# Performance work log

Measured on AMD Instinct MI355X. Metric: run time of the kernel, lower is better.

## Reference

```python
import jax, jax.numpy as jnp
import numpy as np

WS = 8
NH = 6

def _ln(x, g, b, eps=1e-5):
    m = x.mean(-1, keepdims=True)
    v = jnp.var(x, axis=-1, keepdims=True)
    return (x - m) / jnp.sqrt(v + eps) * g + b

def _dwconv(x_nchw, k):
    # depthwise 3x3, stride 1, padding 1 (SAME); k: (C,1,3,3)
    return jax.lax.conv_general_dilated(
        x_nchw, k, (1, 1), 'SAME',
        dimension_numbers=('NCHW', 'OIHW', 'NCHW'),
        feature_group_count=x_nchw.shape[1])

def setup_inputs() -> dict:
    key = jax.random.key(0)
    ks = jax.random.split(key, 12)
    B, H, W, C = 2, 256, 256, 180
    hd_ffn = 360
    s = 0.02
    return {
        'x': jax.random.normal(ks[0], (B, H * W, C), jnp.float32),
        'w_qkv': jax.random.normal(ks[1], (3 * C, C), jnp.float32) * s,
        'b_rel': jax.random.normal(ks[2], (NH, WS * WS, WS * WS), jnp.float32) * s,
        'w_proj': jax.random.normal(ks[3], (C, C), jnp.float32) * s,
        'b_proj': jnp.zeros((C,), jnp.float32),
        'conv_dw': jax.random.normal(ks[4], (C, 1, 3, 3), jnp.float32) * 0.1,
        'cg_w1': jax.random.normal(ks[5], (C // 8, C), jnp.float32) * s,
        'cg_w2': jax.random.normal(ks[6], (C, C // 8), jnp.float32) * s,
        'ffn_w1': jax.random.normal(ks[7], (hd_ffn, C), jnp.float32) * s,
        'ffn_dw': jax.random.normal(ks[8], (hd_ffn, 1, 3, 3), jnp.float32) * 0.1,
        'ffn_w2': jax.random.normal(ks[9], (C, hd_ffn), jnp.float32) * s,
        'n1_g': jnp.ones((C,), jnp.float32),
        'n1_b': jnp.zeros((C,), jnp.float32),
        'n2_g': jnp.ones((C,), jnp.float32),
        'n2_b': jnp.zeros((C,), jnp.float32),
        'H': H,
        'W': W,
    }

def reference(x, w_qkv, b_rel, w_proj, b_proj, conv_dw, cg_w1, cg_w2,
              ffn_w1, ffn_dw, ffn_w2, n1_g, n1_b, n2_g, n2_b, H, W):
    B, L, C = x.shape
    hd = C // NH
    scale = hd ** -0.5
    n1 = _ln(x, n1_g, n1_b)
    # --- spatial window attention branch ---
    xw = n1.reshape(B, H // WS, WS, W // WS, WS, C)
    xw = xw.transpose(0, 1, 3, 2, 4, 5).reshape(-1, WS * WS, C)  # (nw, 64, C)
    qkv = (xw @ w_qkv.T).reshape(-1, WS * WS, 3, NH, hd).transpose(2, 0, 3, 1, 4)
    q, k, v = qkv[0], qkv[1], qkv[2]  # (nw, nh, 64, hd)
    attn = jax.nn.softmax((q * scale) @ jnp.swapaxes(k, -2, -1) + b_rel, axis=-1)
    out = (attn @ v).transpose(0, 2, 1, 3).reshape(-1, WS * WS, C)
    out = out @ w_proj.T + b_proj
    attn_feat = out.reshape(B, H // WS, W // WS, WS, WS, C)
    attn_feat = attn_feat.transpose(0, 1, 3, 2, 4, 5).reshape(B, L, C)
    # --- conv branch: depthwise 3x3 + GELU ---
    nchw = n1.transpose(0, 2, 1).reshape(B, C, H, W)
    conv_feat = jax.nn.gelu(_dwconv(nchw, conv_dw), approximate=False)
    conv_feat = conv_feat.reshape(B, C, L).transpose(0, 2, 1)
    # --- AIM: channel gate on conv_feat modulates attn_feat ---
    pooled = conv_feat.mean(axis=1)  # (B, C) == AdaptiveAvgPool2d(1)
    cm = jax.nn.sigmoid(jax.nn.gelu(pooled @ cg_w1.T, approximate=False) @ cg_w2.T)
    x = x + (attn_feat * cm[:, None, :] + conv_feat)
    # --- FFN with depthwise spatial mixing ---
    n2 = _ln(x, n2_g, n2_b)
    h = jax.nn.gelu(n2 @ ffn_w1.T, approximate=False)  # (B, L, hd_ffn)
    hdim = h.shape[-1]
    h_s = _dwconv(h.transpose(0, 2, 1).reshape(B, hdim, H, W), ffn_dw)
    h_s = h_s.reshape(B, hdim, L).transpose(0, 2, 1)
    return x + h_s @ ffn_w2.T
```

## Files before the change

### kernel.cpp

```cpp
#include <hip/hip_runtime.h>
#include <hip/hip_bf16.h>
#include <math.h>

#define BATCH 2
#define IMG 256
#define LTOK 65536
#define CH 180
#define BL (BATCH * LTOK)
#define HDF 360

using frag_ab = __attribute__((ext_vector_type(8))) short;
using frag_cd = __attribute__((ext_vector_type(4))) float;

__device__ __forceinline__ float b2f(unsigned short u) {
    union { unsigned int i; float f; } v; v.i = ((unsigned int)u) << 16; return v.f;
}
__device__ __forceinline__ float blo(unsigned int u) {
    union { unsigned int i; float f; } v; v.i = u << 16; return v.f;
}
__device__ __forceinline__ float bhi(unsigned int u) {
    union { unsigned int i; float f; } v; v.i = u & 0xffff0000u; return v.f;
}
__device__ __forceinline__ unsigned short f2b(float f) {
    union { float f; unsigned int i; } v; v.f = f;
    unsigned int x = v.i;
    unsigned int r = (x + 0x7fffu + ((x >> 16) & 1u)) >> 16;
    return (unsigned short)r;
}
__device__ __forceinline__ float gelu_f(float x) {
    return 0.5f * x * (1.0f + erff(x * 0.70710678118654752f));
}

template <int PERM>
__device__ __forceinline__ int perm_row(int row) {
    if (PERM == 1) {
        int b = row >> 16, l = row & 65535;
        int y = l >> 8, x = l & 255;
        return (b << 16) + ((((y >> 3) << 5) + (x >> 3)) << 6) + ((y & 7) << 3) + (x & 7);
    } else if (PERM == 2) {
        int b = row >> 16, wv = row & 65535;
        int wid = wv >> 6, t = wv & 63;
        int wy = wid >> 5, wx = wid & 31;
        return (b << 16) + ((((wy << 3) + (t >> 3))) << 8) + (wx << 3) + (t & 7);
    }
    return row;
}

__global__ __launch_bounds__(256) void convw_kernel(
    const float* __restrict__ a, const float* __restrict__ b,
    const float* __restrict__ c, const float* __restrict__ d,
    const float* __restrict__ cdw, const float* __restrict__ fdw,
    unsigned short* __restrict__ wbf, float* __restrict__ wT1, float* __restrict__ wT2)
{
    int g = blockIdx.x * 256 + threadIdx.x;
    if (g < 259200) {
        float v;
        if      (g < 97200)  v = a[g];
        else if (g < 129600) v = b[g - 97200];
        else if (g < 194400) v = c[g - 129600];
        else                 v = d[g - 194400];
        wbf[g] = f2b(v);
    } else if (g < 265680) {
        int i = g - 259200;
        int tap = i / 180, ch = i % 180;
        wT1[i] = cdw[ch * 9 + tap];
    } else if (g < 278640) {
        int i = g - 265680;
        int tap = i / 360, ch = i % 360;
        wT2[i] = fdw[ch * 9 + tap];
    }
}

__device__ __forceinline__ void ld4(const float* p, float v[4]) {
    float4 t = *(const float4*)p; v[0]=t.x; v[1]=t.y; v[2]=t.z; v[3]=t.w;
}
__device__ __forceinline__ void ld4(const unsigned short* p, float v[4]) {
    ushort4 t = *(const ushort4*)p; v[0]=b2f(t.x); v[1]=b2f(t.y); v[2]=b2f(t.z); v[3]=b2f(t.w);
}

template <typename TIN>
__global__ __launch_bounds__(256) void ln_kernel(
    const TIN* __restrict__ x, const float* __restrict__ g,
    const float* __restrict__ bta, unsigned short* __restrict__ out)
{
    int wave = threadIdx.x >> 6, lane = threadIdx.x & 63;
    int tok = blockIdx.x * 4 + wave;
    const bool act = lane < 45;
    float v[4] = {0.f, 0.f, 0.f, 0.f};
    const TIN* row = x + (size_t)tok * CH;
    if (act) ld4(row + lane * 4, v);
    float s  = v[0] + v[1] + v[2] + v[3];
    float sq = v[0]*v[0] + v[1]*v[1] + v[2]*v[2] + v[3]*v[3];
    #pragma unroll
    for (int off = 32; off > 0; off >>= 1) {
        s  += __shfl_xor(s, off);
        sq += __shfl_xor(sq, off);
    }
    float mean = s * (1.f / CH);
    float var  = sq * (1.f / CH) - mean * mean;
    float rstd = rsqrtf(var + 1e-5f);
    if (act) {
        float4 gg = *(const float4*)&g[lane * 4];
        float4 bb = *(const float4*)&bta[lane * 4];
        unsigned int o0 = (unsigned int)f2b((v[0]-mean)*rstd*gg.x + bb.x)
                        | ((unsigned int)f2b((v[1]-mean)*rstd*gg.y + bb.y) << 16);
        unsigned int o1 = (unsigned int)f2b((v[2]-mean)*rstd*gg.z + bb.z)
                        | ((unsigned int)f2b((v[3]-mean)*rstd*gg.w + bb.w) << 16);
        *(uint2*)(out + (size_t)tok * CH + lane * 4) = make_uint2(o0, o1);
    }
}

__device__ __forceinline__ void stv(float* p, float v) { *p = v; }
__device__ __forceinline__ void stv(unsigned short* p, float v) { *p = f2b(v); }

template <int ACT, bool HAS_BIAS, bool HAS_RES, int PERM, typename TOUT>
__global__ __launch_bounds__(256) void gemm_kernel(
    const unsigned short* __restrict__ X, int ldx,
    const unsigned short* __restrict__ Wt,
    const float* __restrict__ bias,
    const unsigned short* __restrict__ res, int ldr,
    TOUT* __restrict__ Y, int ldy,
    int N, int K)
{
    __shared__ unsigned short Xs[64][40];
    __shared__ unsigned short Ws[64][40];
    const int tid = threadIdx.x;
    const int wave = tid >> 6;
    const int lane = tid & 63;
    const int l16 = lane & 15;
    const int q = lane >> 4;
    const int m0 = blockIdx.x * 64;
    const int n0 = blockIdx.y * 64;
    const int lr = tid >> 2;
    const int lk = (tid & 3) << 3;

    frag_cd acc[4];
    #pragma unroll
    for (int i = 0; i < 4; ++i) acc[i] = (frag_cd){0.f, 0.f, 0.f, 0.f};

    for (int k0 = 0; k0 < K; k0 += 32) {
        const bool kfull = (k0 + 32 <= K);
        {
            const unsigned short* p = X + (size_t)(m0 + lr) * ldx + (k0 + lk);
            if (kfull) {
                *(uint2*)&Xs[lr][lk]     = *(const uint2*)p;
                *(uint2*)&Xs[lr][lk + 4] = *(const uint2*)(p + 4);
            } else {
                #pragma unroll
                for (int j = 0; j < 8; ++j)
                    Xs[lr][lk + j] = (k0 + lk + j < K) ? p[j] : (unsigned short)0;
            }
        }
        {
            const int n = n0 + lr;
            const unsigned short* p = Wt + (size_t)n * K + (k0 + lk);
            if (n < N && kfull) {
                *(uint2*)&Ws[lr][lk]     = *(const uint2*)p;
                *(uint2*)&Ws[lr][lk + 4] = *(const uint2*)(p + 4);
            } else {
                #pragma unroll
                for (int j = 0; j < 8; ++j)
                    Ws[lr][lk + j] = (n < N && (k0 + lk + j) < K) ? p[j] : (unsigned short)0;
            }
        }
        __syncthreads();
        frag_ab bfr = *(const frag_ab*)&Ws[wave * 16 + l16][q * 8];
        #pragma unroll
        for (int mb = 0; mb < 4; ++mb) {
            frag_ab afr = *(const frag_ab*)&Xs[mb * 16 + l16][q * 8];
            acc[mb] = __builtin_amdgcn_mfma_f32_16x16x32_bf16(afr, bfr, acc[mb], 0, 0, 0);
        }
        __syncthreads();
    }
    const int col = n0 + wave * 16 + l16;
    if (col < N) {
        float bv = 0.f;
        if (HAS_BIAS) bv = bias[col];
        #pragma unroll
        for (int mb = 0; mb < 4; ++mb) {
            #pragma unroll
            for (int r = 0; r < 4; ++r) {
                int row = m0 + mb * 16 + q * 4 + r;
                int orow = perm_row<PERM>(row);
                float v = acc[mb][r] + bv;
                if (ACT == 1) v = gelu_f(v);
                if (HAS_RES) v += b2f(res[(size_t)orow * ldr + col]);
                stv(&Y[(size_t)orow * ldy + col], v);
            }
        }
    }
}

__global__ __launch_bounds__(64) void attn_kernel(
    const unsigned short* __restrict__ qkvw,
    const float* __restrict__ b_rel,
    unsigned short* __restrict__ attn_out)
{
    __shared__ float kv[64][36];
    const int blk = blockIdx.x;
    const int h = blk % 6;
    const int w = blk / 6;
    const int lane = threadIdx.x;
    const float scale = 0.18257418583505536f;

    const unsigned short* qrow = qkvw + (size_t)(w * 64 + lane) * 540 + h * 30;

    float q[30];
    #pragma unroll
    for (int d = 0; d < 15; ++d) {
        unsigned int u = *(const unsigned int*)(qrow + 2 * d);
        q[2 * d] = blo(u); q[2 * d + 1] = bhi(u);
    }
    #pragma unroll
    for (int d = 0; d < 15; ++d) {
        unsigned int u = *(const unsigned int*)(qrow + 180 + 2 * d);
        kv[lane][2 * d] = blo(u); kv[lane][2 * d + 1] = bhi(u);
    }
    __syncthreads();

    float s[64];
    const float* br = b_rel + h * 4096 + lane * 64;
    #pragma unroll
    for (int j = 0; j < 64; ++j) {
        const float* kj = &kv[j][0];
        float acc = 0.f;
        #pragma unroll
        for (int d = 0; d < 30; ++d) acc += q[d] * kj[d];
        s[j] = acc * scale + br[j];
    }

    float mx = -1e30f;
    #pragma unroll
    for (int j = 0; j < 64; ++j) mx = fmaxf(mx, s[j]);
    float sum = 0.f;
    #pragma unroll
    for (int j = 0; j < 64; ++j) { s[j] = __expf(s[j] - mx); sum += s[j]; }
    float inv = 1.f / sum;

    __syncthreads();
    #pragma unroll
    for (int d = 0; d < 15; ++d) {
        unsigned int u = *(const unsigned int*)(qrow + 360 + 2 * d);
        kv[lane][2 * d] = blo(u); kv[lane][2 * d + 1] = bhi(u);
    }
    __syncthreads();

    float o[30];
    #pragma unroll
    for (int d = 0; d < 30; ++d) o[d] = 0.f;
    #pragma unroll
    for (int j = 0; j < 64; ++j) {
        const float* vj = &kv[j][0];
        float p = s[j];
        #pragma unroll
        for (int d = 0; d < 30; ++d) o[d] += p * vj[d];
    }
    unsigned short* orow = attn_out + (size_t)(w * 64 + lane) * CH + h * 30;
    #pragma unroll
    for (int d = 0; d < 15; ++d) {
        unsigned int u = (unsigned int)f2b(o[2 * d] * inv)
                       | ((unsigned int)f2b(o[2 * d + 1] * inv) << 16);
        *(unsigned int*)(orow + 2 * d) = u;
    }
}

template <int C, bool DO_GELU>
__global__ __launch_bounds__(256) void dwconv_kernel(
    const unsigned short* __restrict__ in, const float* __restrict__ wT,
    unsigned short* __restrict__ out)
{
    constexpr int NG = (C + 7) / 8;
    constexpr int TY = 8;
    int gid = blockIdx.x * 256 + threadIdx.x;
    int cg = gid % NG;
    int t  = gid / NG;
    int x  = t % IMG;
    int t2 = t / IMG;
    int yb = t2 & 31;
    int bi = t2 >> 5;
    if (bi >= BATCH) return;
    const int c0 = cg * 8;
    const int y0 = yb * TY;

    float w9[9][8];
    #pragma unroll
    for (int tp = 0; tp < 9; ++tp) {
        float4 wa = *(const float4*)&wT[tp * C + c0];
        float4 wb = *(const float4*)&wT[tp * C + c0 + 4];
        w9[tp][0]=wa.x; w9[tp][1]=wa.y; w9[tp][2]=wa.z; w9[tp][3]=wa.w;
        w9[tp][4]=wb.x; w9[tp][5]=wb.y; w9[tp][6]=wb.z; w9[tp][7]=wb.w;
    }

    unsigned int rr[3][3][4];

    auto load_row = [&](int y, unsigned int dst[3][4]) {
        if ((unsigned)y >= (unsigned)IMG) {
            #pragma unroll
            for (int cc = 0; cc < 3; ++cc)
                #pragma unroll
                for (int k = 0; k < 4; ++k) dst[cc][k] = 0u;
            return;
        }
        size_t base = ((size_t)((bi << 16) + (y << 8) + x)) * C + c0;
        #pragma unroll
        for (int cc = 0; cc < 3; ++cc) {
            int xx = x + cc - 1;
            if ((unsigned)xx >= (unsigned)IMG) {
                dst[cc][0] = dst[cc][1] = dst[cc][2] = dst[cc][3] = 0u;
                continue;
            }
            const unsigned short* p = in + base + (ptrdiff_t)(cc - 1) * C;
            uint2 u0 = *(const uint2*)p;
            uint2 u1 = *(const uint2*)(p + 4);
            dst[cc][0] = u0.x; dst[cc][1] = u0.y; dst[cc][2] = u1.x; dst[cc][3] = u1.y;
        }
    };

    load_row(y0 - 1, rr[0]);
    load_row(y0,     rr[1]);

    #pragma unroll
    for (int dy = 0; dy < TY; ++dy) {
        load_row(y0 + dy + 1, rr[(dy + 2) % 3]);
        float acc[8];
        #pragma unroll
        for (int j = 0; j < 8; ++j) acc[j] = 0.f;
        #pragma unroll
        for (int ky = 0; ky < 3; ++ky) {
            unsigned int (*row)[4] = rr[(dy + ky) % 3];
            #pragma unroll
            for (int kx = 0; kx < 3; ++kx) {
                const float* wp = w9[ky * 3 + kx];
                const unsigned int* u = row[kx];
                acc[0] += blo(u[0]) * wp[0];
                acc[1] += bhi(u[0]) * wp[1];
                acc[2] += blo(u[1]) * wp[2];
                acc[3] += bhi(u[1]) * wp[3];
                acc[4] += blo(u[2]) * wp[4];
                acc[5] += bhi(u[2]) * wp[5];
                acc[6] += blo(u[3]) * wp[6];
                acc[7] += bhi(u[3]) * wp[7];
            }
        }
        if (DO_GELU) {
            #pragma unroll
            for (int j = 0; j < 8; ++j) acc[j] = gelu_f(acc[j]);
        }
        size_t ob = ((size_t)((bi << 16) + ((y0 + dy) << 8) + x)) * C + c0;
        unsigned int o0 = (unsigned int)f2b(acc[0]) | ((unsigned int)f2b(acc[1]) << 16);
        unsigned int o1 = (unsigned int)f2b(acc[2]) | ((unsigned int)f2b(acc[3]) << 16);
        *(uint2*)(out + ob) = make_uint2(o0, o1);
        if (c0 + 8 <= C) {
            unsigned int o2 = (unsigned int)f2b(acc[4]) | ((unsigned int)f2b(acc[5]) << 16);
            unsigned int o3 = (unsigned int)f2b(acc[6]) | ((unsigned int)f2b(acc[7]) << 16);
            *(uint2*)(out + ob + 4) = make_uint2(o2, o3);
        }
    }
}

__global__ __launch_bounds__(64) void pool_kernel(
    const unsigned short* __restrict__ cf, float* __restrict__ pooled)
{
    int t = threadIdx.x;
    if (t >= 45) return;
    int b = blockIdx.x >> 7;
    int chunk = blockIdx.x & 127;
    const unsigned short* base = cf + (size_t)(b * LTOK + chunk * 512) * CH + t * 4;
    float s0 = 0.f, s1 = 0.f, s2 = 0.f, s3 = 0.f;
    for (int i = 0; i < 512; ++i) {
        ushort4 v = *(const ushort4*)(base + (size_t)i * CH);
        s0 += b2f(v.x); s1 += b2f(v.y); s2 += b2f(v.z); s3 += b2f(v.w);
    }
    atomicAdd(&pooled[b * CH + t * 4 + 0], s0);
    atomicAdd(&pooled[b * CH + t * 4 + 1], s1);
    atomicAdd(&pooled[b * CH + t * 4 + 2], s2);
    atomicAdd(&pooled[b * CH + t * 4 + 3], s3);
}

__global__ __launch_bounds__(256) void cm_kernel(
    const float* __restrict__ pooled, const float* __restrict__ w1,
    const float* __restrict__ w2, float* __restrict__ cm)
{
    __shared__ float p[BATCH][CH];
    __shared__ float g1[BATCH][22];
    int t = threadIdx.x;
    for (int idx = t; idx < BATCH * CH; idx += 256)
        p[idx / CH][idx % CH] = pooled[idx] * (1.f / (float)LTOK);
    __syncthreads();
    if (t < BATCH * 22) {
        int b = t / 22, u = t % 22;
        float s = 0.f;
        for (int c = 0; c < CH; ++c) s += p[b][c] * w1[u * CH + c];
        g1[b][u] = gelu_f(s);
    }
    __syncthreads();
    for (int idx = t; idx < BATCH * CH; idx += 256) {
        int b = idx / CH, c = idx % CH;
        float s = 0.f;
        for (int u = 0; u < 22; ++u) s += g1[b][u] * w2[c * 22 + u];
        cm[idx] = 1.f / (1.f + __expf(-s));
    }
}

__global__ __launch_bounds__(256) void resid_kernel(
    const float* __restrict__ x, const unsigned short* __restrict__ attn_feat,
    const unsigned short* __restrict__ conv_feat, const float* __restrict__ cm,
    unsigned short* __restrict__ x_mid)
{
    int gid = blockIdx.x * 256 + threadIdx.x;
    int c4 = gid % 45;
    int b = gid / (LTOK * 45);
    float4 xv = ((const float4*)x)[gid];
    ushort4 a = ((const ushort4*)attn_feat)[gid];
    ushort4 c = ((const ushort4*)conv_feat)[gid];
    float4 m = *(const float4*)&cm[b * CH + c4 * 4];
    unsigned int o0 = (unsigned int)f2b(xv.x + b2f(a.x) * m.x + b2f(c.x))
                    | ((unsigned int)f2b(xv.y + b2f(a.y) * m.y + b2f(c.y)) << 16);
    unsigned int o1 = (unsigned int)f2b(xv.z + b2f(a.z) * m.z + b2f(c.z))
                    | ((unsigned int)f2b(xv.w + b2f(a.w) * m.w + b2f(c.w)) << 16);
    ((uint2*)x_mid)[gid] = make_uint2(o0, o1);
}

extern "C" void kernel_launch(void* const* d_in, const int* in_sizes, int n_in,
                              void* d_out, int out_size, void* d_ws, size_t ws_size,
                              hipStream_t stream)
{
    const float* x       = (const float*)d_in[0];
    const float* w_qkv   = (const float*)d_in[1];
    const float* b_rel   = (const float*)d_in[2];
    const float* w_proj  = (const float*)d_in[3];
    const float* b_proj  = (const float*)d_in[4];
    const float* conv_dw = (const float*)d_in[5];
    const float* cg_w1   = (const float*)d_in[6];
    const float* cg_w2   = (const float*)d_in[7];
    const float* ffn_w1  = (const float*)d_in[8];
    const float* ffn_dw  = (const float*)d_in[9];
    const float* ffn_w2  = (const float*)d_in[10];
    const float* n1_g    = (const float*)d_in[11];
    const float* n1_b    = (const float*)d_in[12];
    const float* n2_g    = (const float*)d_in[13];
    const float* n2_b    = (const float*)d_in[14];

    char* ws = (char*)d_ws;
    unsigned short* n1        = (unsigned short*)(ws);
    unsigned short* qkvw      = (unsigned short*)(ws + 47185920);
    unsigned short* conv_feat = (unsigned short*)(ws + 188743680);
    unsigned short* attn_out  = (unsigned short*)(ws);
    unsigned short* attn_feat = (unsigned short*)(ws + 47185920);
    unsigned short* x_mid     = (unsigned short*)(ws + 94371840);
    unsigned short* n2        = (unsigned short*)(ws + 141557760);
    unsigned short* h         = (unsigned short*)(ws);
    unsigned short* h_s       = (unsigned short*)(ws + 141557760);
    float*          pooled    = (float*)(ws + 235929600);
    float*          cmv       = (float*)(ws + 235931040);
    unsigned short* wbf       = (unsigned short*)(ws + 235932480);
    float*          wT1       = (float*)(ws + 236450880);
    float*          wT2       = (float*)(ws + 236476800);
    unsigned short* wqkv_b  = wbf;
    unsigned short* wproj_b = wbf + 97200;
    unsigned short* wffn1_b = wbf + 129600;
    unsigned short* wffn2_b = wbf + 194400;
    float* out = (float*)d_out;

    hipMemsetAsync(pooled, 0, 2880, stream);

    convw_kernel<<<1089, 256, 0, stream>>>(w_qkv, w_proj, ffn_w1, ffn_w2,
                                           conv_dw, ffn_dw, wbf, wT1, wT2);
    ln_kernel<float><<<BL / 4, 256, 0, stream>>>(x, n1_g, n1_b, n1);
    gemm_kernel<0, false, false, 1, unsigned short><<<dim3(BL / 64, 9), 256, 0, stream>>>(
        n1, CH, wqkv_b, nullptr, nullptr, 0, qkvw, 540, 540, CH);
    dwconv_kernel<CH, true><<<1472, 256, 0, stream>>>(n1, wT1, conv_feat);
    pool_kernel<<<BATCH * 128, 64, 0, stream>>>(conv_feat, pooled);
    cm_kernel<<<1, 256, 0, stream>>>(pooled, cg_w1, cg_w2, cmv);
    attn_kernel<<<2048 * 6, 64, 0, stream>>>(qkvw, b_rel, attn_out);
    gemm_kernel<0, true, false, 2, unsigned short><<<dim3(BL / 64, 3), 256, 0, stream>>>(
        attn_out, CH, wproj_b, b_proj, nullptr, 0, attn_feat, CH, CH, CH);
    resid_kernel<<<(BL * CH / 4) / 256, 256, 0, stream>>>(x, attn_feat, conv_feat, cmv, x_mid);
    ln_kernel<unsigned short><<<BL / 4, 256, 0, stream>>>(x_mid, n2_g, n2_b, n2);
    gemm_kernel<1, false, false, 0, unsigned short><<<dim3(BL / 64, 6), 256, 0, stream>>>(
        n2, CH, wffn1_b, nullptr, nullptr, 0, h, HDF, HDF, CH);
    dwconv_kernel<HDF, false><<<2880, 256, 0, stream>>>(h, wT2, h_s);
    gemm_kernel<0, false, true, 0, float><<<dim3(BL / 64, 3), 256, 0, stream>>>(
        h_s, HDF, wffn2_b, nullptr, x_mid, CH, out, CH, CH, HDF);
}
```

Baseline: 1.063 ms.

## Compute window attention with bf16 MFMA and pre-swizzled relative bias

Rewrites the per-window attention kernel to compute QK^T and PV using 16x16x32 bf16 MFMA instructions instead of scalar FP32 dot products, with the softmax done in the MFMA accumulator layout using cross-lane shuffles. The relative position bias is converted once to bf16 and permuted into the accumulator fragment layout in the weight-conversion kernel, so each thread loads its bias values with wide vector loads. Probabilities are rounded to bf16 before the PV product and the bias is held at bf16 precision, which loosens accuracy slightly. The head dimension of 30 is zero-padded to 32 for the MFMA.

```diff
diff --git a/kernel.cpp b/kernel.cpp
--- a/kernel.cpp
+++ b/kernel.cpp
@@ -50,7 +50,9 @@
     const float* __restrict__ a, const float* __restrict__ b,
     const float* __restrict__ c, const float* __restrict__ d,
     const float* __restrict__ cdw, const float* __restrict__ fdw,
-    unsigned short* __restrict__ wbf, float* __restrict__ wT1, float* __restrict__ wT2)
+    const float* __restrict__ brel,
+    unsigned short* __restrict__ wbf, float* __restrict__ wT1, float* __restrict__ wT2,
+    unsigned short* __restrict__ br3)
 {
     int g = blockIdx.x * 256 + threadIdx.x;
     if (g < 259200) {
@@ -68,6 +70,16 @@
         int i = g - 265680;
         int tap = i / 360, ch = i % 360;
         wT2[i] = fdw[ch * 9 + tap];
+    } else if (g < 303216) {
+        int i = g - 278640;
+        int h = i >> 12;
+        int rem = i & 4095;
+        int lane = rem >> 6;
+        int j = rem & 63;
+        int mt = j >> 4, nt = (j >> 2) & 3, r = j & 3;
+        int row = mt * 16 + (lane >> 4) * 4 + r;
+        int col = nt * 16 + (lane & 15);
+        br3[i] = f2b(brel[h * 4096 + row * 64 + col]);
     }
 }
 
@@ -193,74 +205,132 @@
 
 __global__ __launch_bounds__(64) void attn_kernel(
     const unsigned short* __restrict__ qkvw,
-    const float* __restrict__ b_rel,
+    const unsigned short* __restrict__ br3,
     unsigned short* __restrict__ attn_out)
 {
-    __shared__ float kv[64][36];
+    __shared__ unsigned short Pl[64][72];
+    __shared__ unsigned short VT[32][72];
     const int blk = blockIdx.x;
     const int h = blk % 6;
     const int w = blk / 6;
     const int lane = threadIdx.x;
+    const int l16 = lane & 15;
+    const int g4 = lane >> 4;
     const float scale = 0.18257418583505536f;
 
-    const unsigned short* qrow = qkvw + (size_t)(w * 64 + lane) * 540 + h * 30;
-
-    float q[30];
-    #pragma unroll
-    for (int d = 0; d < 15; ++d) {
-        unsigned int u = *(const unsigned int*)(qrow + 2 * d);
-        q[2 * d] = blo(u); q[2 * d + 1] = bhi(u);
-    }
-    #pragma unroll
-    for (int d = 0; d < 15; ++d) {
-        unsigned int u = *(const unsigned int*)(qrow + 180 + 2 * d);
-        kv[lane][2 * d] = blo(u); kv[lane][2 * d + 1] = bhi(u);
+    const unsigned short* base = qkvw + (size_t)w * (64 * 540) + h * 30;
+
+    frag_ab qf[4], kf[4];
+    #pragma unroll
+    for (int t = 0; t < 4; ++t) {
+        const unsigned short* pq = base + (size_t)(t * 16 + l16) * 540 + g4 * 8;
+        union { frag_ab f; uint2 u[2]; } tq, tk;
+        tq.u[0] = *(const uint2*)pq;        tq.u[1] = *(const uint2*)(pq + 4);
+        tk.u[0] = *(const uint2*)(pq + 180); tk.u[1] = *(const uint2*)(pq + 184);
+        if (g4 == 3) { tk.f[6] = 0; tk.f[7] = 0; }
+        qf[t] = tq.f; kf[t] = tk.f;
+    }
+
+    unsigned int brw[32];
+    {
+        const unsigned short* bp = br3 + ((size_t)h << 12) + lane * 64;
+        #pragma unroll
+        for (int c2 = 0; c2 < 8; ++c2)
+            *(uint4*)&brw[c2 * 4] = *(const uint4*)(bp + c2 * 8);
+    }
+
+    frag_cd s[4][4];
+    #pragma unroll
+    for (int mt = 0; mt < 4; ++mt)
+        #pragma unroll
+        for (int nt = 0; nt < 4; ++nt)
+            s[mt][nt] = (frag_cd){0.f, 0.f, 0.f, 0.f};
+    #pragma unroll
+    for (int mt = 0; mt < 4; ++mt)
+        #pragma unroll
+        for (int nt = 0; nt < 4; ++nt)
+            s[mt][nt] = __builtin_amdgcn_mfma_f32_16x16x32_bf16(qf[mt], kf[nt], s[mt][nt], 0, 0, 0);
+
+    {
+        const unsigned short* pv = base + (size_t)lane * 540 + 360;
+        #pragma unroll
+        for (int d2 = 0; d2 < 15; ++d2) {
+            unsigned int u = *(const unsigned int*)(pv + 2 * d2);
+            VT[2 * d2][lane]     = (unsigned short)(u & 0xffffu);
+            VT[2 * d2 + 1][lane] = (unsigned short)(u >> 16);
+        }
+        VT[30][lane] = 0; VT[31][lane] = 0;
+    }
+
+    float inv[4][4];
+    #pragma unroll
+    for (int mt = 0; mt < 4; ++mt) {
+        #pragma unroll
+        for (int r = 0; r < 4; ++r) {
+            float a0 = s[mt][0][r] * scale + (((0 * 4 + r) & 1) ? bhi(brw[(mt * 16 + 0 + r) >> 1]) : blo(brw[(mt * 16 + 0 + r) >> 1]));
+            float a1 = s[mt][1][r] * scale + (((1 * 4 + r) & 1) ? bhi(brw[(mt * 16 + 4 + r) >> 1]) : blo(brw[(mt * 16 + 4 + r) >> 1]));
+            float a2 = s[mt][2][r] * scale + (((2 * 4 + r) & 1) ? bhi(brw[(mt * 16 + 8 + r) >> 1]) : blo(brw[(mt * 16 + 8 + r) >> 1]));
+            float a3 = s[mt][3][r] * scale + (((3 * 4 + r) & 1) ? bhi(brw[(mt * 16 + 12 + r) >> 1]) : blo(brw[(mt * 16 + 12 + r) >> 1]));
+            float m = fmaxf(fmaxf(a0, a1), fmaxf(a2, a3));
+            m = fmaxf(m, __shfl_xor(m, 1));
+            m = fmaxf(m, __shfl_xor(m, 2));
+            m = fmaxf(m, __shfl_xor(m, 4));
+            m = fmaxf(m, __shfl_xor(m, 8));
+            float e0 = __expf(a0 - m), e1 = __expf(a1 - m);
+            float e2 = __expf(a2 - m), e3 = __expf(a3 - m);
+            float sum = e0 + e1 + e2 + e3;
+            sum += __shfl_xor(sum, 1);
+            sum += __shfl_xor(sum, 2);
+            sum += __shfl_xor(sum, 4);
+            sum += __shfl_xor(sum, 8);
+            inv[mt][r] = 1.f / sum;
+            int row = mt * 16 + g4 * 4 + r;
+            Pl[row][l16]      = f2b(e0);
+            Pl[row][16 + l16] = f2b(e1);
+            Pl[row][32 + l16] = f2b(e2);
+            Pl[row][48 + l16] = f2b(e3);
+        }
     }
     __syncthreads();
 
-    float s[64];
-    const float* br = b_rel + h * 4096 + lane * 64;
-    #pragma unroll
-    for (int j = 0; j < 64; ++j) {
-        const float* kj = &kv[j][0];
-        float acc = 0.f;
-        #pragma unroll
-        for (int d = 0; d < 30; ++d) acc += q[d] * kj[d];
-        s[j] = acc * scale + br[j];
-    }
-
-    float mx = -1e30f;
-    #pragma unroll
-    for (int j = 0; j < 64; ++j) mx = fmaxf(mx, s[j]);
-    float sum = 0.f;
-    #pragma unroll
-    for (int j = 0; j < 64; ++j) { s[j] = __expf(s[j] - mx); sum += s[j]; }
-    float inv = 1.f / sum;
-
-    __syncthreads();
-    #pragma unroll
-    for (int d = 0; d < 15; ++d) {
-        unsigned int u = *(const unsigned int*)(qrow + 360 + 2 * d);
-        kv[lane][2 * d] = blo(u); kv[lane][2 * d + 1] = bhi(u);
-    }
-    __syncthreads();
-
-    float o[30];
-    #pragma unroll
-    for (int d = 0; d < 30; ++d) o[d] = 0.f;
-    #pragma unroll
-    for (int j = 0; j < 64; ++j) {
-        const float* vj = &kv[j][0];
-        float p = s[j];
-        #pragma unroll
-        for (int d = 0; d < 30; ++d) o[d] += p * vj[d];
-    }
-    unsigned short* orow = attn_out + (size_t)(w * 64 + lane) * CH + h * 30;
-    #pragma unroll
-    for (int d = 0; d < 15; ++d) {
-        unsigned int u = (unsigned int)f2b(o[2 * d] * inv)
-                       | ((unsigned int)f2b(o[2 * d + 1] * inv) << 16);
-        *(unsigned int*)(orow + 2 * d) = u;
+    frag_ab pf[4][2];
+    #pragma unroll
+    for (int mt = 0; mt < 4; ++mt)
+        #pragma unroll
+        for (int kt = 0; kt < 2; ++kt)
+            pf[mt][kt] = *(const frag_ab*)&Pl[mt * 16 + l16][kt * 32 + g4 * 8];
+    frag_ab vf[2][2];
+    #pragma unroll
+    for (int nt = 0; nt < 2; ++nt)
+        #pragma unroll
+        for (int kt = 0; kt < 2; ++kt)
+            vf[nt][kt] = *(const frag_ab*)&VT[nt * 16 + l16][kt * 32 + g4 * 8];
+
+    frag_cd o[4][2];
+    #pragma unroll
+    for (int mt = 0; mt < 4; ++mt)
+        #pragma unroll
+        for (int nt = 0; nt < 2; ++nt)
+            o[mt][nt] = (frag_cd){0.f, 0.f, 0.f, 0.f};
+    #pragma unroll
+    for (int mt = 0; mt < 4; ++mt)
+        #pragma unroll
+        for (int nt = 0; nt < 2; ++nt)
+            #pragma unroll
+            for (int kt = 0; kt < 2; ++kt)
+                o[mt][nt] = __builtin_amdgcn_mfma_f32_16x16x32_bf16(pf[mt][kt], vf[nt][kt], o[mt][nt], 0, 0, 0);
+
+    unsigned short* ob = attn_out + (size_t)w * (64 * CH) + h * 30;
+    #pragma unroll
+    for (int mt = 0; mt < 4; ++mt) {
+        #pragma unroll
+        for (int r = 0; r < 4; ++r) {
+            int row = mt * 16 + g4 * 4 + r;
+            float iv = inv[mt][r];
+            unsigned short* op = ob + (size_t)row * CH;
+            op[l16] = f2b(o[mt][0][r] * iv);
+            if (l16 < 14) op[16 + l16] = f2b(o[mt][1][r] * iv);
+        }
     }
 }
 
@@ -456,6 +526,7 @@
     unsigned short* wbf       = (unsigned short*)(ws + 235932480);
     float*          wT1       = (float*)(ws + 236450880);
     float*          wT2       = (float*)(ws + 236476800);
+    unsigned short* br3       = (unsigned short*)(ws + 236528640);
     unsigned short* wqkv_b  = wbf;
     unsigned short* wproj_b = wbf + 97200;
     unsigned short* wffn1_b = wbf + 129600;
@@ -464,15 +535,15 @@
 
     hipMemsetAsync(pooled, 0, 2880, stream);
 
-    convw_kernel<<<1089, 256, 0, stream>>>(w_qkv, w_proj, ffn_w1, ffn_w2,
-                                           conv_dw, ffn_dw, wbf, wT1, wT2);
+    convw_kernel<<<1185, 256, 0, stream>>>(w_qkv, w_proj, ffn_w1, ffn_w2,
+                                           conv_dw, ffn_dw, b_rel, wbf, wT1, wT2, br3);
     ln_kernel<float><<<BL / 4, 256, 0, stream>>>(x, n1_g, n1_b, n1);
     gemm_kernel<0, false, false, 1, unsigned short><<<dim3(BL / 64, 9), 256, 0, stream>>>(
         n1, CH, wqkv_b, nullptr, nullptr, 0, qkvw, 540, 540, CH);
     dwconv_kernel<CH, true><<<1472, 256, 0, stream>>>(n1, wT1, conv_feat);
     pool_kernel<<<BATCH * 128, 64, 0, stream>>>(conv_feat, pooled);
     cm_kernel<<<1, 256, 0, stream>>>(pooled, cg_w1, cg_w2, cmv);
-    attn_kernel<<<2048 * 6, 64, 0, stream>>>(qkvw, b_rel, attn_out);
+    attn_kernel<<<2048 * 6, 64, 0, stream>>>(qkvw, br3, attn_out);
     gemm_kernel<0, true, false, 2, unsigned short><<<dim3(BL / 64, 3), 256, 0, stream>>>(
         attn_out, CH, wproj_b, b_proj, nullptr, 0, attn_feat, CH, CH, CH);
     resid_kernel<<<(BL * CH / 4) / 256, 256, 0, stream>>>(x, attn_feat, conv_feat, cmv, x_mid);
```

After: 952.5 us. 10.4% less time.
